# Kernel tuning notes

Hardware: AMD Instinct MI355X
Metric: run time of the kernel (lower is better)

The kernel has to match this reference:

```python
import jax, jax.numpy as jnp
import numpy as np

HIDDEN = 128
GLOBAL_HIDDEN = 128
STATE_DIM = 8
FEATURE = HIDDEN + GLOBAL_HIDDEN + STATE_DIM  # 264, as in SympleAgent.feature_size
NUM_OPS = 30
NUM_INTERNAL_OPS = 5
N_NODES = 400000


def _ffn(x, W1, b1, W2, b2):
    # FFN(in, hidden, out, n_layers=1): Linear -> ReLU -> Linear
    return jax.nn.relu(x @ W1 + b1) @ W2 + b2


def setup_inputs() -> dict:
    key = jax.random.key(0)
    ks = jax.random.split(key, 20)
    s = 0.02

    def lin(k, fan_in, fan_out):
        k1, k2 = jax.random.split(k)
        return (jax.random.normal(k1, (fan_in, fan_out), jnp.float32) * s,
                jax.random.normal(k2, (fan_out,), jnp.float32) * s)

    W_hl1, b_hl1 = lin(ks[0], FEATURE, HIDDEN)
    W_hl2, b_hl2 = lin(ks[1], HIDDEN, 4)            # high_level_actor -> 4
    W_in1, b_in1 = lin(ks[2], FEATURE, HIDDEN)
    W_in2, b_in2 = lin(ks[3], HIDDEN, NUM_INTERNAL_OPS)  # internal_actor
    W_ex1, b_ex1 = lin(ks[4], FEATURE, HIDDEN)
    W_ex2, b_ex2 = lin(ks[5], HIDDEN, NUM_OPS)      # actor (external ops)
    W_tp1, b_tp1 = lin(ks[6], FEATURE, HIDDEN)
    W_tp2, b_tp2 = lin(ks[7], HIDDEN, 1)            # teleport_ffn -> 1 per node

    node_hidden = jax.random.normal(ks[8], (N_NODES, HIDDEN), jnp.float32)
    h_glob = jax.random.normal(ks[9], (1, GLOBAL_HIDDEN), jnp.float32)
    state_tensor = jax.random.normal(ks[10], (1, STATE_DIM), jnp.float32)
    validity_mask = jnp.ones((1, NUM_OPS), jnp.float32)

    return {
        "node_hidden": node_hidden, "h_glob": h_glob,
        "state_tensor": state_tensor, "validity_mask": validity_mask,
        "W_hl1": W_hl1, "b_hl1": b_hl1, "W_hl2": W_hl2, "b_hl2": b_hl2,
        "W_in1": W_in1, "b_in1": b_in1, "W_in2": W_in2, "b_in2": b_in2,
        "W_ex1": W_ex1, "b_ex1": b_ex1, "W_ex2": W_ex2, "b_ex2": b_ex2,
        "W_tp1": W_tp1, "b_tp1": b_tp1, "W_tp2": W_tp2, "b_tp2": b_tp2,
    }


def reference(node_hidden, h_glob, state_tensor, validity_mask,
              W_hl1, b_hl1, W_hl2, b_hl2,
              W_in1, b_in1, W_in2, b_in2,
              W_ex1, b_ex1, W_ex2, b_ex2,
              W_tp1, b_tp1, W_tp2, b_tp2):
    # --- get_policy_logits for current node (coord -> node 0) ---
    cur = node_hidden[0:1]                                   # [1, H]
    feats = jnp.concatenate([cur, h_glob, state_tensor], -1)  # [1, FEATURE]
    l_high = _ffn(feats, W_hl1, b_hl1, W_hl2, b_hl2)          # [1, 4]
    l_internal = _ffn(feats, W_in1, b_in1, W_in2, b_in2)      # [1, 5]
    l_ext = _ffn(feats, W_ex1, b_ex1, W_ex2, b_ex2) + jnp.log(validity_mask)  # [1, NUM_OPS]

    # --- apply_teleport_ffn: features over all n_nodes ---
    n = node_hidden.shape[0]
    hg = jnp.broadcast_to(h_glob, (n, h_glob.shape[-1]))      # h_glob[-1].repeat(n,1)
    st = jnp.broadcast_to(state_tensor, (n, state_tensor.shape[-1]))
    tp_feats = jnp.concatenate([hg, node_hidden, st], -1)     # [n, FEATURE]
    l_teleport = _ffn(tp_feats, W_tp1, b_tp1, W_tp2, b_tp2).T  # [1, n]

    # concatenate all heads along the logit axis: [1, 4 + 5 + NUM_OPS + n]
    return jnp.concatenate([l_high, l_internal, l_ext, l_teleport], axis=-1)
```

## Files before the change

### kernel.cpp

```cpp
#include <hip/hip_runtime.h>
#include <hip/hip_bf16.h>
#include <stdint.h>

typedef __attribute__((ext_vector_type(8))) short short8;
typedef __bf16 bf16x8 __attribute__((ext_vector_type(8)));
typedef __attribute__((ext_vector_type(4))) float f32x4;

#define HID 128
#define NTILES 8
#define KSTEPS 4

#define WS_C_F    8192
#define WS_W2_F   8320
#define WS_B2_F   8448

#define TP_BLOCKS   256
#define TP_WAVES    7
#define TP_THREADS  (TP_WAVES * 64)
#define TOTAL_TP_WAVES (TP_BLOCKS * TP_WAVES)

#define SLOT_BYTES    8192
#define WEIGHTS_BYTES 33792
#define SMEM_BYTES    (WEIGHTS_BYTES + TP_WAVES * 2 * SLOT_BYTES)

__global__ void prep_kernel(const float* __restrict__ node_hidden,
                            const float* __restrict__ h_glob,
                            const float* __restrict__ state,
                            const float* __restrict__ validity,
                            const float* __restrict__ W_hl1, const float* __restrict__ b_hl1,
                            const float* __restrict__ W_hl2, const float* __restrict__ b_hl2,
                            const float* __restrict__ W_in1, const float* __restrict__ b_in1,
                            const float* __restrict__ W_in2, const float* __restrict__ b_in2,
                            const float* __restrict__ W_ex1, const float* __restrict__ b_ex1,
                            const float* __restrict__ W_ex2, const float* __restrict__ b_ex2,
                            const float* __restrict__ W_tp1, const float* __restrict__ b_tp1,
                            const float* __restrict__ W_tp2, const float* __restrict__ b_tp2,
                            float* __restrict__ out, float* __restrict__ ws)
{
    const int tid = threadIdx.x;
    const int b = blockIdx.x;

    if (b < 3) {
        __shared__ float feats[264];
        __shared__ float hidden[128];
        const float* W1 = (b == 0) ? W_hl1 : (b == 1 ? W_in1 : W_ex1);
        const float* b1 = (b == 0) ? b_hl1 : (b == 1 ? b_in1 : b_ex1);
        const float* W2 = (b == 0) ? W_hl2 : (b == 1 ? W_in2 : W_ex2);
        const float* b2 = (b == 0) ? b_hl2 : (b == 1 ? b_in2 : b_ex2);
        const int od    = (b == 0) ? 4 : (b == 1 ? 5 : 30);
        const int obase = (b == 0) ? 0 : (b == 1 ? 4 : 9);

        for (int i = tid; i < 264; i += 256) {
            float v;
            if (i < 128)      v = node_hidden[i];
            else if (i < 256) v = h_glob[i - 128];
            else              v = state[i - 256];
            feats[i] = v;
        }
        __syncthreads();
        if (tid < 128) {
            float h = b1[tid];
            for (int i = 0; i < 264; ++i) h += feats[i] * W1[i * 128 + tid];
            hidden[tid] = fmaxf(h, 0.f);
        }
        __syncthreads();
        if (tid < od) {
            float o = b2[tid];
            for (int i = 0; i < 128; ++i) o += hidden[i] * W2[i * od + tid];
            if (b == 2) o += logf(validity[tid]);
            out[obase + tid] = o;
        }
    } else if (b == 3) {
        if (tid < 128) {
            float c = b_tp1[tid];
            for (int i = 0; i < 128; ++i) c += h_glob[i] * W_tp1[i * HID + tid];
            for (int i = 0; i < 8;  ++i)  c += state[i] * W_tp1[(256 + i) * HID + tid];
            ws[WS_C_F  + tid] = c;
            ws[WS_W2_F + tid] = W_tp2[tid];
            if (tid == 0) ws[WS_B2_F] = b_tp2[0];
        }
    } else {
        short* afrag = (short*)ws;
        const int part = b - 4;
        for (int idx = part * 1024 + tid; idx < part * 1024 + 1024; idx += 256) {
            const int k = idx >> 7, nn = idx & 127;
            const int t = nn >> 4, cc = nn & 15;
            const int s = k >> 5, rr = k & 31;
            const int g = rr >> 3, j = rr & 7;
            const int lane = cc + (g << 4);
            afrag[(((t * KSTEPS + s) * 64 + lane) << 3) + j] =
                (short)__builtin_bit_cast(unsigned short, (__bf16)W_tp1[(128 + k) * HID + nn]);
        }
    }
}

__launch_bounds__(TP_THREADS)
__global__ void teleport_kernel(const float* __restrict__ node_hidden,
                                const float* __restrict__ ws,
                                float* __restrict__ out,
                                int n)
{
    __shared__ __align__(16) unsigned char smem[SMEM_BYTES];
    const int tid = threadIdx.x;

    {
        const int4* wsv = (const int4*)ws;
        int4* sv = (int4*)smem;
        for (int i = tid; i < 2112; i += TP_THREADS) sv[i] = wsv[i];
    }
    const float bias2 = ws[WS_B2_F];
    __syncthreads();

    const short* afrag  = (const short*)smem;
    const float* c_all  = (const float*)(smem + 32768);
    const float* w2_all = (const float*)(smem + 33280);

    const int lane = tid & 63;
    const int wave = tid >> 6;
    const int m  = lane & 15;
    const int g  = lane >> 4;
    const unsigned mx = (unsigned)(m & 7);
    const unsigned mrow = (unsigned)m * 512;

    unsigned char* slotA = smem + WEIGHTS_BYTES + wave * 2 * SLOT_BYTES;
    unsigned char* slotB = slotA + SLOT_BYTES;

    const int nChunks = (n + 15) >> 4;
    const int gw = blockIdx.x * TP_WAVES + wave;
    const int c0 = (int)(((long long)gw * nChunks) / TOTAL_TP_WAVES);
    const int c1 = (int)(((long long)(gw + 1) * nChunks) / TOTAL_TP_WAVES);

#define STAGE(slot_, c_)                                                         \
    {                                                                            \
        _Pragma("unroll")                                                        \
        for (int k_ = 0; k_ < 8; ++k_) {                                         \
            const int row_ = 2 * k_ + (lane >> 5);                               \
            const int grow_ = min((c_) * 16 + row_, n - 1);                      \
            const unsigned su_ = ((unsigned)(lane & 31)) ^ ((unsigned)(row_ & 7));\
            const unsigned char* src_ = (const unsigned char*)node_hidden        \
                                        + (size_t)grow_ * 512 + (su_ << 4);      \
            __builtin_amdgcn_global_load_lds(                                    \
                (const __attribute__((address_space(1))) unsigned int*)src_,     \
                (__attribute__((address_space(3))) unsigned int*)(slot_ + k_ * 1024), \
                16, 0, 0);                                                       \
        }                                                                        \
    }

    if (c0 < c1) {
        STAGE(slotA, c0);
        if (c0 + 1 < c1) STAGE(slotB, c0 + 1);
        unsigned char* cur = slotA;
        unsigned char* nxt = slotB;

        for (int c = c0; c < c1; ++c) {
            if (c + 1 < c1) {
                asm volatile("s_waitcnt vmcnt(8)" ::: "memory");
            } else {
                asm volatile("s_waitcnt vmcnt(0)" ::: "memory");
            }

            bf16x8 nd[KSTEPS];
            #pragma unroll
            for (int s = 0; s < KSTEPS; ++s) {
                const unsigned u0 = (((unsigned)(s * 8 + g * 2))     ^ mx) << 4;
                const unsigned u1 = (((unsigned)(s * 8 + g * 2 + 1)) ^ mx) << 4;
                const float4 fa = *(const float4*)(cur + mrow + u0);
                const float4 fb = *(const float4*)(cur + mrow + u1);
                bf16x8 a;
                a[0] = (__bf16)fa.x; a[1] = (__bf16)fa.y; a[2] = (__bf16)fa.z; a[3] = (__bf16)fa.w;
                a[4] = (__bf16)fb.x; a[5] = (__bf16)fb.y; a[6] = (__bf16)fb.z; a[7] = (__bf16)fb.w;
                nd[s] = a;
            }
            __builtin_amdgcn_sched_barrier(0);
            if (c + 2 < c1) STAGE(cur, c + 2);

            float sr = 0.f;
            #pragma unroll
            for (int t = 0; t < NTILES; ++t) {
                f32x4 acc = (f32x4){0.f, 0.f, 0.f, 0.f};
                #pragma unroll
                for (int s = 0; s < KSTEPS; ++s) {
                    const short8 wv = *(const short8*)&afrag[(((t * KSTEPS + s) * 64 + lane) << 3)];
                    const bf16x8 wf = __builtin_bit_cast(bf16x8, wv);
                    acc = __builtin_amdgcn_mfma_f32_16x16x32_bf16(wf, nd[s], acc, 0, 0, 0);
                }
                const float4 c4 = *(const float4*)(c_all  + t * 16 + g * 4);
                const float4 w4 = *(const float4*)(w2_all + t * 16 + g * 4);
                float h0 = acc[0] + c4.x, h1 = acc[1] + c4.y;
                float h2 = acc[2] + c4.z, h3 = acc[3] + c4.w;
                h0 = h0 > 0.f ? h0 : 0.f;  h1 = h1 > 0.f ? h1 : 0.f;
                h2 = h2 > 0.f ? h2 : 0.f;  h3 = h3 > 0.f ? h3 : 0.f;
                sr += h0 * w4.x + h1 * w4.y + h2 * w4.z + h3 * w4.w;
            }

            sr += __shfl_xor(sr, 16, 64);
            sr += __shfl_xor(sr, 32, 64);

            if (lane < 16) {
                const int o = c * 16 + lane;
                if (o < n) out[o] = sr + bias2;
            }

            unsigned char* tmp = cur; cur = nxt; nxt = tmp;
        }
    }
#undef STAGE
}

extern "C" void kernel_launch(void* const* d_in, const int* in_sizes, int n_in,
                              void* d_out, int out_size, void* d_ws, size_t ws_size,
                              hipStream_t stream) {
    const float* node_hidden = (const float*)d_in[0];
    const float* h_glob      = (const float*)d_in[1];
    const float* state       = (const float*)d_in[2];
    const float* validity    = (const float*)d_in[3];
    const float* W_hl1 = (const float*)d_in[4];  const float* b_hl1 = (const float*)d_in[5];
    const float* W_hl2 = (const float*)d_in[6];  const float* b_hl2 = (const float*)d_in[7];
    const float* W_in1 = (const float*)d_in[8];  const float* b_in1 = (const float*)d_in[9];
    const float* W_in2 = (const float*)d_in[10]; const float* b_in2 = (const float*)d_in[11];
    const float* W_ex1 = (const float*)d_in[12]; const float* b_ex1 = (const float*)d_in[13];
    const float* W_ex2 = (const float*)d_in[14]; const float* b_ex2 = (const float*)d_in[15];
    const float* W_tp1 = (const float*)d_in[16]; const float* b_tp1 = (const float*)d_in[17];
    const float* W_tp2 = (const float*)d_in[18]; const float* b_tp2 = (const float*)d_in[19];

    float* out = (float*)d_out;
    float* ws  = (float*)d_ws;
    const int n = in_sizes[0] / HID;

    prep_kernel<<<20, 256, 0, stream>>>(node_hidden, h_glob, state, validity,
                                        W_hl1, b_hl1, W_hl2, b_hl2,
                                        W_in1, b_in1, W_in2, b_in2,
                                        W_ex1, b_ex1, W_ex2, b_ex2,
                                        W_tp1, b_tp1, W_tp2, b_tp2,
                                        out, ws);
    teleport_kernel<<<TP_BLOCKS, TP_THREADS, 0, stream>>>(node_hidden, ws, out + 39, n);
}
```

Measured before the change: 53.18 us.

## Triple-buffer teleport LDS staging with fewer waves and parallelize prep GEMVs

The teleport kernel moves from 7 waves with double-buffered LDS slots to 5 waves with three slots each, prefetching three chunks ahead and adjusting the vmcnt waits to match. This gives each wave more loads in flight to hide global memory latency, at the cost of fewer waves per block. The prep kernel now runs with 512 threads and splits the 264- and 136-long dot products across four thread groups, reducing its serial latency. The vmcnt thresholds are tuned by hand and have to match the number of outstanding loads exactly, including the output stores, which adds fragility.

```diff
diff --git a/kernel.cpp b/kernel.cpp
--- a/kernel.cpp
+++ b/kernel.cpp
@@ -15,13 +15,13 @@
 #define WS_B2_F   8448
 
 #define TP_BLOCKS   256
-#define TP_WAVES    7
+#define TP_WAVES    5
 #define TP_THREADS  (TP_WAVES * 64)
 #define TOTAL_TP_WAVES (TP_BLOCKS * TP_WAVES)
 
 #define SLOT_BYTES    8192
 #define WEIGHTS_BYTES 33792
-#define SMEM_BYTES    (WEIGHTS_BYTES + TP_WAVES * 2 * SLOT_BYTES)
+#define SMEM_BYTES    (WEIGHTS_BYTES + TP_WAVES * 3 * SLOT_BYTES)
 
 __global__ void prep_kernel(const float* __restrict__ node_hidden,
                             const float* __restrict__ h_glob,
@@ -42,6 +42,7 @@
 
     if (b < 3) {
         __shared__ float feats[264];
+        __shared__ float hpart[4][128];
         __shared__ float hidden[128];
         const float* W1 = (b == 0) ? W_hl1 : (b == 1 ? W_in1 : W_ex1);
         const float* b1 = (b == 0) ? b_hl1 : (b == 1 ? b_in1 : b_ex1);
@@ -50,17 +51,23 @@
         const int od    = (b == 0) ? 4 : (b == 1 ? 5 : 30);
         const int obase = (b == 0) ? 0 : (b == 1 ? 4 : 9);
 
-        for (int i = tid; i < 264; i += 256) {
+        if (tid < 264) {
             float v;
-            if (i < 128)      v = node_hidden[i];
-            else if (i < 256) v = h_glob[i - 128];
-            else              v = state[i - 256];
-            feats[i] = v;
+            if (tid < 128)      v = node_hidden[tid];
+            else if (tid < 256) v = h_glob[tid - 128];
+            else                v = state[tid - 256];
+            feats[tid] = v;
+        }
+        __syncthreads();
+        {
+            const int j = tid & 127, q = tid >> 7;
+            float s = 0.f;
+            for (int i = q * 66; i < q * 66 + 66; ++i) s += feats[i] * W1[i * 128 + j];
+            hpart[q][j] = s;
         }
         __syncthreads();
         if (tid < 128) {
-            float h = b1[tid];
-            for (int i = 0; i < 264; ++i) h += feats[i] * W1[i * 128 + tid];
+            float h = b1[tid] + hpart[0][tid] + hpart[1][tid] + hpart[2][tid] + hpart[3][tid];
             hidden[tid] = fmaxf(h, 0.f);
         }
         __syncthreads();
@@ -71,18 +78,26 @@
             out[obase + tid] = o;
         }
     } else if (b == 3) {
+        __shared__ float cpart[4][128];
+        {
+            const int j = tid & 127, q = tid >> 7;
+            float s = 0.f;
+            for (int i = q * 32; i < q * 32 + 32; ++i) s += h_glob[i] * W_tp1[i * HID + j];
+            if (q == 3)
+                for (int i = 0; i < 8; ++i) s += state[i] * W_tp1[(256 + i) * HID + j];
+            cpart[q][j] = s;
+        }
+        __syncthreads();
         if (tid < 128) {
-            float c = b_tp1[tid];
-            for (int i = 0; i < 128; ++i) c += h_glob[i] * W_tp1[i * HID + tid];
-            for (int i = 0; i < 8;  ++i)  c += state[i] * W_tp1[(256 + i) * HID + tid];
-            ws[WS_C_F  + tid] = c;
+            ws[WS_C_F  + tid] = b_tp1[tid] + cpart[0][tid] + cpart[1][tid]
+                                           + cpart[2][tid] + cpart[3][tid];
             ws[WS_W2_F + tid] = W_tp2[tid];
             if (tid == 0) ws[WS_B2_F] = b_tp2[0];
         }
     } else {
         short* afrag = (short*)ws;
         const int part = b - 4;
-        for (int idx = part * 1024 + tid; idx < part * 1024 + 1024; idx += 256) {
+        for (int idx = part * 1024 + tid; idx < part * 1024 + 1024; idx += 512) {
             const int k = idx >> 7, nn = idx & 127;
             const int t = nn >> 4, cc = nn & 15;
             const int s = k >> 5, rr = k & 31;
@@ -122,8 +137,9 @@
     const unsigned mx = (unsigned)(m & 7);
     const unsigned mrow = (unsigned)m * 512;
 
-    unsigned char* slotA = smem + WEIGHTS_BYTES + wave * 2 * SLOT_BYTES;
-    unsigned char* slotB = slotA + SLOT_BYTES;
+    unsigned char* p0 = smem + WEIGHTS_BYTES + wave * 3 * SLOT_BYTES;
+    unsigned char* p1 = p0 + SLOT_BYTES;
+    unsigned char* p2 = p1 + SLOT_BYTES;
 
     const int nChunks = (n + 15) >> 4;
     const int gw = blockIdx.x * TP_WAVES + wave;
@@ -147,13 +163,15 @@
     }
 
     if (c0 < c1) {
-        STAGE(slotA, c0);
-        if (c0 + 1 < c1) STAGE(slotB, c0 + 1);
-        unsigned char* cur = slotA;
-        unsigned char* nxt = slotB;
+        STAGE(p0, c0);
+        if (c0 + 1 < c1) STAGE(p1, c0 + 1);
+        if (c0 + 2 < c1) STAGE(p2, c0 + 2);
 
         for (int c = c0; c < c1; ++c) {
-            if (c + 1 < c1) {
+            if (c + 3 <= c1) {
+                if (c >= c0 + 3) { asm volatile("s_waitcnt vmcnt(19)" ::: "memory"); }
+                else             { asm volatile("s_waitcnt vmcnt(16)" ::: "memory"); }
+            } else if (c + 2 == c1) {
                 asm volatile("s_waitcnt vmcnt(8)" ::: "memory");
             } else {
                 asm volatile("s_waitcnt vmcnt(0)" ::: "memory");
@@ -164,15 +182,15 @@
             for (int s = 0; s < KSTEPS; ++s) {
                 const unsigned u0 = (((unsigned)(s * 8 + g * 2))     ^ mx) << 4;
                 const unsigned u1 = (((unsigned)(s * 8 + g * 2 + 1)) ^ mx) << 4;
-                const float4 fa = *(const float4*)(cur + mrow + u0);
-                const float4 fb = *(const float4*)(cur + mrow + u1);
+                const float4 fa = *(const float4*)(p0 + mrow + u0);
+                const float4 fb = *(const float4*)(p0 + mrow + u1);
                 bf16x8 a;
                 a[0] = (__bf16)fa.x; a[1] = (__bf16)fa.y; a[2] = (__bf16)fa.z; a[3] = (__bf16)fa.w;
                 a[4] = (__bf16)fb.x; a[5] = (__bf16)fb.y; a[6] = (__bf16)fb.z; a[7] = (__bf16)fb.w;
                 nd[s] = a;
             }
             __builtin_amdgcn_sched_barrier(0);
-            if (c + 2 < c1) STAGE(cur, c + 2);
+            if (c + 3 < c1) STAGE(p0, c + 3);
 
             float sr = 0.f;
             #pragma unroll
@@ -201,7 +219,7 @@
                 if (o < n) out[o] = sr + bias2;
             }
 
-            unsigned char* tmp = cur; cur = nxt; nxt = tmp;
+            unsigned char* tmp = p0; p0 = p1; p1 = p2; p2 = tmp;
         }
     }
 #undef STAGE
@@ -227,7 +245,7 @@
     float* ws  = (float*)d_ws;
     const int n = in_sizes[0] / HID;
 
-    prep_kernel<<<20, 256, 0, stream>>>(node_hidden, h_glob, state, validity,
+    prep_kernel<<<20, 512, 0, stream>>>(node_hidden, h_glob, state, validity,
                                         W_hl1, b_hl1, W_hl2, b_hl2,
                                         W_in1, b_in1, W_in2, b_in2,
                                         W_ex1, b_ex1, W_ex2, b_ex2,
```

Measured after the change: 52.20 us. About the same (-1.8%).
